# Performance work log

Hardware: AMD Instinct MI355X
Metric: run time of the kernel (lower is better)

## Reference

```python
import jax, jax.numpy as jnp
import numpy as np


def _find(parent, x):
    # chase parent pointers to the root (root = min-rank node of its component)
    return jax.lax.while_loop(lambda v: parent[v] != v, lambda v: parent[v], x)


def _pd0_single(fcol, src, dst):
    """0-dim persistence diagram for one filtration column.

    Semantics match TOGL.generate_persistence_diagram_dim0:
      - nodes are added in sorted order of fcol; birth(node) = its sorted rank
      - directed edge (u, v) merges components at step rank(v) iff rank(u) < rank(v)
      - elder rule: the component whose root has the larger rank dies
      - output row i = (birth=i, death) for the node of rank i (insertion order of
        the original dict is exactly rank order); death = inf for survivors.
    """
    n = fcol.shape[0]
    order = jnp.argsort(fcol)
    rank = jnp.zeros((n,), jnp.int32).at[order].set(jnp.arange(n, dtype=jnp.int32))
    a = rank[src]                      # rank-space endpoints
    b = rank[dst]
    valid = a < b                      # only edges whose source is already active fire
    w = jnp.where(valid, b, n)         # edge weight = step at which it fires
    perm = jnp.argsort(w)              # Kruskal order
    ea, eb, ev = a[perm], b[perm], valid[perm]

    def step(carry, e):
        parent, deaths = carry
        ia, ib, v = e
        ra = _find(parent, ia)
        rb = _find(parent, ib)
        merge = v & (ra != rb)
        elder = jnp.minimum(ra, rb)
        younger = jnp.maximum(ra, rb)
        deaths = deaths.at[younger].set(jnp.where(merge, ib.astype(deaths.dtype), deaths[younger]))
        parent = parent.at[younger].set(jnp.where(merge, elder, parent[younger]))
        # path compression at the two queried nodes
        parent = parent.at[ia].set(jnp.where(merge, elder, ra))
        parent = parent.at[ib].set(jnp.where(merge, elder, rb))
        return (parent, deaths), None

    parent0 = jnp.arange(n, dtype=jnp.int32)
    deaths0 = jnp.full((n,), jnp.inf, jnp.float32)
    (parent, deaths), _ = jax.lax.scan(step, (parent0, deaths0), (ea, eb, ev))
    births = jnp.arange(n, dtype=jnp.float32)
    return jnp.stack([births, deaths], axis=1)  # (n_nodes, 2)


def setup_inputs() -> dict:
    key = jax.random.key(0)
    k = jax.random.split(key, 6)
    N, F, H, NF, E = 20000, 1024, 2048, 4, 160000
    X = jax.random.normal(k[0], (N, F), jnp.float32)
    edge_index = jax.random.randint(k[1], (2, E), 0, N, jnp.int64)
    W1 = jax.random.normal(k[2], (F, H), jnp.float32) / np.sqrt(F)
    b1 = jax.random.normal(k[3], (H,), jnp.float32) * 0.01
    W2 = jax.random.normal(k[4], (H, NF), jnp.float32) / np.sqrt(H)
    b2 = jax.random.normal(k[5], (NF,), jnp.float32) * 0.01
    return {"X": X, "edge_index": edge_index, "W1": W1, "b1": b1, "W2": W2, "b2": b2}


def reference(X, edge_index, W1, b1, W2, b2):
    # filter_graph: Linear -> ReLU -> Linear
    filt = jnp.maximum(X @ W1 + b1, 0.0) @ W2 + b2            # (N, n_filtrations)
    src = edge_index[0].astype(jnp.int32)
    dst = edge_index[1].astype(jnp.int32)
    diagrams = jax.vmap(_pd0_single, in_axes=(1, None, None))(filt, src, dst)  # (NF, N, 2)
    return filt, diagrams
```

## Files before the change

### kernel.cpp

```cpp
#include <hip/hip_runtime.h>

typedef unsigned long long u64;
typedef unsigned int u32;
typedef unsigned short ushort_t;
typedef __attribute__((ext_vector_type(8))) short short8;
typedef __attribute__((ext_vector_type(4))) float fx4;

#define F_DIM 1024
#define H_DIM 2048
#define NFOUT 4
#define WS_W1T_OFF (1u << 20)

__device__ __forceinline__ ushort_t f2bf(float x)
{
    union { float f; u32 u; } c; c.f = x;
    u32 b = c.u;
    u32 r = b + 0x7FFFu + ((b >> 16) & 1u);
    return (ushort_t)(r >> 16);
}
__device__ __forceinline__ float bf2f(ushort_t h)
{
    union { u32 u; float f; } c; c.u = ((u32)h) << 16;
    return c.f;
}
__device__ __forceinline__ void split3(float x, ushort_t& u0, ushort_t& u1, ushort_t& u2)
{
    u0 = f2bf(x);
    float r1 = x - bf2f(u0);
    u1 = f2bf(r1);
    float r2 = r1 - bf2f(u1);
    u2 = f2bf(r2);
}

__global__ __launch_bounds__(256)
void k_w1split(const float* __restrict__ W1, ushort_t* __restrict__ w1t)
{
    __shared__ __align__(16) ushort_t LT[3][64][72];
    const int t = threadIdx.x;
    const int bk = blockIdx.x >> 5;
    const int bh = blockIdx.x & 31;
    const int k0 = bk * 64, h0 = bh * 64;
    const int kk = t >> 4, hb = (t & 15) * 4;
    #pragma unroll
    for (int j = 0; j < 4; j++) {
        int row = kk + j * 16;
        float4 v = *(const float4*)(W1 + (size_t)(k0 + row) * H_DIM + h0 + hb);
        float xs[4] = { v.x, v.y, v.z, v.w };
        #pragma unroll
        for (int c = 0; c < 4; c++) {
            ushort_t u0, u1, u2;
            split3(xs[c], u0, u1, u2);
            LT[0][hb + c][row] = u0;
            LT[1][hb + c][row] = u1;
            LT[2][hb + c][row] = u2;
        }
    }
    __syncthreads();
    const int hl = t >> 2, sg = t & 3;
    #pragma unroll
    for (int p = 0; p < 3; p++)
        #pragma unroll
        for (int q = 0; q < 2; q++) {
            int ks = sg * 16 + q * 8;
            *(short8*)(w1t + (size_t)p * (H_DIM * (size_t)F_DIM)
                       + (size_t)(h0 + hl) * F_DIM + k0 + ks) =
                *(const short8*)&LT[p][hl][ks];
        }
}

__device__ __forceinline__ fx4 mfma16(short8 a, short8 b, fx4 c)
{
    return __builtin_amdgcn_mfma_f32_16x16x32_bf16(a, b, c, 0, 0, 0);
}

#define AP_BYTES (3 * 64 * 128)
#define BP_BYTES (3 * 256 * 128)
#define SM_BYTES (AP_BYTES + BP_BYTES + 256 * 4 * 4)
#define HPITCH 261

__global__ __launch_bounds__(512, 2)
void k_filt_mfma(const float* __restrict__ X, const ushort_t* __restrict__ w1t,
                 const float* __restrict__ b1, const float* __restrict__ W2,
                 const float* __restrict__ b2, float* __restrict__ out, int N)
{
    extern __shared__ char smem[];
    char* Ac = smem;
    char* Bc = smem + AP_BYTES;
    float* W2s = (float*)(smem + AP_BYTES + BP_BYTES);
    float* hid = (float*)Bc;
    float* part = (float*)Ac;

    const int t = threadIdx.x;
    const int lane = t & 63;
    const int w = t >> 6;
    const int wr = (w & 1) * 32;
    const int wc = (w >> 1) * 64;
    const int r0 = blockIdx.x * 64;
    const int l15 = lane & 15, l4 = lane >> 4;

    const int arow = t >> 3;
    const int ak8  = (t & 7) * 8;
    const bool arow_ok = (r0 + arow) < N;
    const int brow = t >> 1;
    const int bseg = (t & 1) * 64;

    const int g2row = lane;
    const int g2nf  = w & 3;
    const int g2seg = w >> 2;

    float Afl[8];
    short8 Bv[12];
    fx4 acc[2][4];
    float pacc = 0.f;
    #pragma unroll
    for (int i = 0; i < 2; i++)
        #pragma unroll
        for (int j = 0; j < 4; j++) acc[i][j] = (fx4)(0.f);

    {
        if (arow_ok) {
            float4 v0 = *(const float4*)(X + (size_t)(r0 + arow) * F_DIM + ak8);
            float4 v1 = *(const float4*)(X + (size_t)(r0 + arow) * F_DIM + ak8 + 4);
            Afl[0] = v0.x; Afl[1] = v0.y; Afl[2] = v0.z; Afl[3] = v0.w;
            Afl[4] = v1.x; Afl[5] = v1.y; Afl[6] = v1.z; Afl[7] = v1.w;
        } else {
            #pragma unroll
            for (int j = 0; j < 8; j++) Afl[j] = 0.f;
        }
        #pragma unroll
        for (int p = 0; p < 3; p++)
            #pragma unroll
            for (int q = 0; q < 4; q++)
                Bv[p * 4 + q] = *(const short8*)(w1t + (size_t)p * (H_DIM * (size_t)F_DIM)
                                 + (size_t)brow * F_DIM + (bseg + q * 16) / 2);
    }

    for (int it = 0; it < 128; ++it) {
        const int hc = it >> 4, kc = it & 15;

        ushort_t s0[8], s1[8], s2[8];
        #pragma unroll
        for (int j = 0; j < 8; j++) split3(Afl[j], s0[j], s1[j], s2[j]);
        short8 Au0, Au1, Au2;
        #pragma unroll
        for (int j = 0; j < 8; j++) { Au0[j] = (short)s0[j]; Au1[j] = (short)s1[j]; Au2[j] = (short)s2[j]; }

        __syncthreads();

        {
            const int aswz = (arow & 7) << 4;
            const int abyte = (ak8 * 2);
            *(short8*)(Ac + 0 * 8192 + arow * 128 + (abyte ^ aswz)) = Au0;
            *(short8*)(Ac + 1 * 8192 + arow * 128 + (abyte ^ aswz)) = Au1;
            *(short8*)(Ac + 2 * 8192 + arow * 128 + (abyte ^ aswz)) = Au2;
            const int bswz = (brow & 7) << 4;
            #pragma unroll
            for (int p = 0; p < 3; p++)
                #pragma unroll
                for (int q = 0; q < 4; q++)
                    *(short8*)(Bc + p * 32768 + brow * 128 + ((bseg + q * 16) ^ bswz)) = Bv[p * 4 + q];
            if (kc == 0 && t < 256)
                *(float4*)&W2s[t * 4] = *(const float4*)(W2 + ((size_t)hc * 256 + t) * NFOUT);
        }

        if (it + 1 < 128) {
            const int hn = (it + 1) >> 4, kn = (it + 1) & 15;
            if (arow_ok) {
                float4 v0 = *(const float4*)(X + (size_t)(r0 + arow) * F_DIM + kn * 64 + ak8);
                float4 v1 = *(const float4*)(X + (size_t)(r0 + arow) * F_DIM + kn * 64 + ak8 + 4);
                Afl[0] = v0.x; Afl[1] = v0.y; Afl[2] = v0.z; Afl[3] = v0.w;
                Afl[4] = v1.x; Afl[5] = v1.y; Afl[6] = v1.z; Afl[7] = v1.w;
            }
            #pragma unroll
            for (int p = 0; p < 3; p++)
                #pragma unroll
                for (int q = 0; q < 4; q++)
                    Bv[p * 4 + q] = *(const short8*)(w1t + (size_t)p * (H_DIM * (size_t)F_DIM)
                                     + (size_t)(hn * 256 + brow) * F_DIM + kn * 64 + (bseg + q * 16) / 2);
        }

        __syncthreads();

        #pragma unroll
        for (int sub = 0; sub < 2; ++sub) {
            const int kb = sub * 64 + l4 * 16;
            const int sw = (l15 & 7) << 4;
            short8 a[2][3];
            #pragma unroll
            for (int rr = 0; rr < 2; ++rr) {
                const int row = wr + rr * 16 + l15;
                #pragma unroll
                for (int p = 0; p < 3; p++)
                    a[rr][p] = *(const short8*)(Ac + p * 8192 + row * 128 + (kb ^ sw));
            }
            #pragma unroll
            for (int cf = 0; cf < 4; ++cf) {
                const int hrow = wc + cf * 16 + l15;
                short8 bb0 = *(const short8*)(Bc + 0 * 32768 + hrow * 128 + (kb ^ sw));
                short8 bb1 = *(const short8*)(Bc + 1 * 32768 + hrow * 128 + (kb ^ sw));
                short8 bb2 = *(const short8*)(Bc + 2 * 32768 + hrow * 128 + (kb ^ sw));
                #pragma unroll
                for (int rr = 0; rr < 2; ++rr) {
                    fx4 c = acc[rr][cf];
                    c = mfma16(a[rr][0], bb0, c);
                    c = mfma16(a[rr][0], bb1, c);
                    c = mfma16(a[rr][1], bb0, c);
                    c = mfma16(a[rr][0], bb2, c);
                    c = mfma16(a[rr][1], bb1, c);
                    c = mfma16(a[rr][2], bb0, c);
                    acc[rr][cf] = c;
                }
            }
        }

        if (kc == 15) {
            __syncthreads();
            #pragma unroll
            for (int rr = 0; rr < 2; ++rr)
                #pragma unroll
                for (int cf = 0; cf < 4; ++cf) {
                    const int hl = wc + cf * 16 + l15;
                    const float bias1 = b1[hc * 256 + hl];
                    #pragma unroll
                    for (int g = 0; g < 4; g++) {
                        const int rl = wr + rr * 16 + l4 * 4 + g;
                        hid[rl * HPITCH + hl] = fmaxf(acc[rr][cf][g] + bias1, 0.f);
                    }
                    acc[rr][cf] = (fx4)(0.f);
                }
            __syncthreads();
            {
                const float* hp = hid + g2row * HPITCH + g2seg * 128;
                const int hb = g2seg * 128;
                #pragma unroll 16
                for (int j = 0; j < 128; j++)
                    pacc = fmaf(hp[j], W2s[(hb + j) * 4 + g2nf], pacc);
            }
        }
    }

    __syncthreads();
    part[g2row * 8 + g2nf * 2 + g2seg] = pacc;
    __syncthreads();
    if (t < 256) {
        const int row = t >> 2, nf = t & 3;
        const float s = part[row * 8 + nf * 2 + 0] + part[row * 8 + nf * 2 + 1];
        const int rg = r0 + row;
        if (rg < N) out[(size_t)rg * NFOUT + nf] = s + b2[nf];
    }
}

#define BM 64
#define BH 64
#define KCH 64
#define LROW 68

__global__ __launch_bounds__(256, 2)
void k_filt(const float* __restrict__ X, const float* __restrict__ W1,
            const float* __restrict__ b1, const float* __restrict__ W2,
            const float* __restrict__ b2, float* __restrict__ out, int N)
{
    __shared__ float Xs[KCH * LROW];
    __shared__ float Ws[KCH * LROW];
    __shared__ float W2s[BH * NFOUT];
    const int t = threadIdx.x;
    const int r0 = blockIdx.x * BM;
    const int tr = t >> 4, tc = t & 15;
    const int orow = t >> 2, onf = t & 3;
    float fchain = 0.0f;
    for (int hc = 0; hc < H_DIM; hc += BH) {
        float acc[4][4];
        #pragma unroll
        for (int i = 0; i < 4; i++)
            #pragma unroll
            for (int j = 0; j < 4; j++) acc[i][j] = 0.0f;
        for (int kc = 0; kc < F_DIM; kc += KCH) {
            {
                const int rowq = t >> 4, kkq = t & 15;
                float xv[4][4];
                #pragma unroll
                for (int j = 0; j < 4; j++) {
                    int r = r0 + rowq * 4 + j;
                    float4 v = (r < N) ? *(const float4*)(X + (size_t)r * F_DIM + kc + kkq * 4)
                                       : make_float4(0.f, 0.f, 0.f, 0.f);
                    xv[j][0] = v.x; xv[j][1] = v.y; xv[j][2] = v.z; xv[j][3] = v.w;
                }
                #pragma unroll
                for (int j = 0; j < 4; j++)
                    *(float4*)&Xs[(kkq * 4 + j) * LROW + rowq * 4] =
                        make_float4(xv[0][j], xv[1][j], xv[2][j], xv[3][j]);
            }
            {
                const int hq = t & 15;
                #pragma unroll
                for (int q = 0; q < 4; q++) {
                    int kk = (t >> 4) + q * 16;
                    *(float4*)&Ws[kk * LROW + hq * 4] =
                        *(const float4*)(W1 + (size_t)(kc + kk) * H_DIM + hc + hq * 4);
                }
            }
            __syncthreads();
            #pragma unroll 8
            for (int kk = 0; kk < KCH; kk++) {
                float4 xv = *(float4*)&Xs[kk * LROW + tr * 4];
                float4 wv = *(float4*)&Ws[kk * LROW + tc * 4];
                acc[0][0] = fmaf(xv.x, wv.x, acc[0][0]); acc[0][1] = fmaf(xv.x, wv.y, acc[0][1]);
                acc[0][2] = fmaf(xv.x, wv.z, acc[0][2]); acc[0][3] = fmaf(xv.x, wv.w, acc[0][3]);
                acc[1][0] = fmaf(xv.y, wv.x, acc[1][0]); acc[1][1] = fmaf(xv.y, wv.y, acc[1][1]);
                acc[1][2] = fmaf(xv.y, wv.z, acc[1][2]); acc[1][3] = fmaf(xv.y, wv.w, acc[1][3]);
                acc[2][0] = fmaf(xv.z, wv.x, acc[2][0]); acc[2][1] = fmaf(xv.z, wv.y, acc[2][1]);
                acc[2][2] = fmaf(xv.z, wv.z, acc[2][2]); acc[2][3] = fmaf(xv.z, wv.w, acc[2][3]);
                acc[3][0] = fmaf(xv.w, wv.x, acc[3][0]); acc[3][1] = fmaf(xv.w, wv.y, acc[3][1]);
                acc[3][2] = fmaf(xv.w, wv.z, acc[3][2]); acc[3][3] = fmaf(xv.w, wv.w, acc[3][3]);
            }
            __syncthreads();
        }
        {
            float4 bv = *(const float4*)(b1 + hc + tc * 4);
            #pragma unroll
            for (int i = 0; i < 4; i++) {
                float4 hv;
                hv.x = fmaxf(acc[i][0] + bv.x, 0.f);
                hv.y = fmaxf(acc[i][1] + bv.y, 0.f);
                hv.z = fmaxf(acc[i][2] + bv.z, 0.f);
                hv.w = fmaxf(acc[i][3] + bv.w, 0.f);
                *(float4*)&Ws[(tr * 4 + i) * LROW + tc * 4] = hv;
            }
            if (t < BH)
                *(float4*)&W2s[t * 4] = *(const float4*)(W2 + (size_t)(hc + t) * NFOUT);
        }
        __syncthreads();
        #pragma unroll 16
        for (int hh = 0; hh < BH; hh++)
            fchain = fmaf(Ws[orow * LROW + hh], W2s[hh * 4 + onf], fchain);
        __syncthreads();
    }
    {
        int r = r0 + orow;
        if (r < N) out[(size_t)r * NFOUT + onf] = fchain + b2[onf];
    }
}

__global__ void k_prep(u32* __restrict__ rank, int N)
{
    int g = blockIdx.x * blockDim.x + threadIdx.x;
    if (g < 4 * N) rank[g] = 0u;
}

#define JTILE 2048

__global__ __launch_bounds__(256)
void k_rank(const float* __restrict__ filt, u32* __restrict__ rank,
            int N, int nchunk)
{
    __shared__ float4 lds[JTILE];
    const int chunk = blockIdx.x % nchunk;
    const int jslice = blockIdx.x / nchunk;
    const int jt = jslice * JTILE;
    const int i = chunk * 256 + threadIdx.x;
    const bool iok = i < N;
    float4 vi = iok ? *(const float4*)(filt + (size_t)i * 4)
                    : make_float4(0.f, 0.f, 0.f, 0.f);
    for (int s = 0; s < JTILE; s += 256) {
        int j = jt + s + threadIdx.x;
        lds[s + threadIdx.x] = (j < N)
            ? *(const float4*)(filt + (size_t)j * 4)
            : make_float4(INFINITY, INFINITY, INFINITY, INFINITY);
    }
    __syncthreads();
    int c0 = 0, c1 = 0, c2 = 0, c3 = 0;
    #pragma unroll 4
    for (int jj = 0; jj < JTILE; jj++) {
        float4 vj = lds[jj];
        int j = jt + jj;
        bool jlt = j < i;
        c0 += (vj.x < vi.x) || (vj.x == vi.x && jlt);
        c1 += (vj.y < vi.y) || (vj.y == vi.y && jlt);
        c2 += (vj.z < vi.z) || (vj.z == vi.z && jlt);
        c3 += (vj.w < vi.w) || (vj.w == vi.w && jlt);
    }
    if (iok) {
        atomicAdd(&rank[0 * N + i], (u32)c0);
        atomicAdd(&rank[1 * N + i], (u32)c1);
        atomicAdd(&rank[2 * N + i], (u32)c2);
        atomicAdd(&rank[3 * N + i], (u32)c3);
    }
}

__device__ __forceinline__ u32 lds_aload(u32* p)
{
    return __hip_atomic_load(p, __ATOMIC_RELAXED, __HIP_MEMORY_SCOPE_WORKGROUP);
}

__device__ __forceinline__ u32 rep_walk32(u32* S, u32 u, u32 t, u32& sv_out)
{
    u32 sv = lds_aload(&S[u]);
    while ((sv >> 16) <= t) {
        u = sv & 0xFFFFu;
        sv = lds_aload(&S[u]);
    }
    sv_out = sv;
    return u;
}

__device__ void do_merge32(u32* S, u32 u, u32 v, u32 t)
{
    for (int guard = 0; guard < (1 << 22); guard++) {
        u32 svu, svv;
        u = rep_walk32(S, u, t, svu);
        v = rep_walk32(S, v, t, svv);
        if (u == v) return;
        if (u < v) { u32 tm = u; u = v; v = tm; u32 ts = svu; svu = svv; svv = ts; }
        u32 s = svu >> 16;
        if (s <= t) continue;
        u32 des = (t << 16) | v;
        u32 old = atomicCAS(&S[u], svu, des);
        if (old == svu) {
            if (s == 0xFFFFu) return;
            u = v; v = old & 0xFFFFu;
            t = s;
        }
    }
}

__global__ __launch_bounds__(1024, 1)
void k_merge4(const int* __restrict__ eidx, const u32* __restrict__ rank,
              float* __restrict__ dg, int N, int E)
{
    extern __shared__ u32 S[];
    const int f = blockIdx.x;
    const u32* rk = rank + (size_t)f * N;

    for (int u = threadIdx.x; u < N; u += blockDim.x)
        S[u] = (0xFFFFu << 16) | (u32)u;
    __syncthreads();

    for (int e = threadIdx.x; e < E; e += blockDim.x) {
        u32 a = rk[eidx[e]];
        u32 b = rk[eidx[E + e]];
        if (a < b) do_merge32(S, a, b, b);
    }
    __syncthreads();

    for (int r = threadIdx.x; r < N; r += blockDim.x) {
        u32 s = S[r] >> 16;
        float death = (s == 0xFFFFu) ? 3.0e38f : (float)s;
        dg[(size_t)f * N * 2 + (size_t)r * 2 + 0] = (float)r;
        dg[(size_t)f * N * 2 + (size_t)r * 2 + 1] = death;
    }
}

extern "C" void kernel_launch(void* const* d_in, const int* in_sizes, int n_in,
                              void* d_out, int out_size, void* d_ws, size_t ws_size,
                              hipStream_t stream)
{
    const float* X  = (const float*)d_in[0];
    const int*   EI = (const int*)d_in[1];
    const float* W1 = (const float*)d_in[2];
    const float* b1 = (const float*)d_in[3];
    const float* W2 = (const float*)d_in[4];
    const float* b2 = (const float*)d_in[5];
    const int N = in_sizes[0] / F_DIM;
    const int E = in_sizes[1] / 2;

    float* out = (float*)d_out;
    float* dg  = out + (size_t)N * NFOUT;
    u32* rank  = (u32*)d_ws;

    static bool attr_set = false;
    if (!attr_set) {
        (void)hipFuncSetAttribute((const void*)k_merge4,
                                  hipFuncAttributeMaxDynamicSharedMemorySize,
                                  160 * 1024);
        (void)hipFuncSetAttribute((const void*)k_filt_mfma,
                                  hipFuncAttributeMaxDynamicSharedMemorySize,
                                  160 * 1024);
        attr_set = true;
    }

    k_prep<<<(4 * N + 255) / 256, 256, 0, stream>>>(rank, N);

    const size_t w1t_need = (size_t)WS_W1T_OFF + 3ull * H_DIM * F_DIM * 2;
    if (ws_size >= w1t_need) {
        ushort_t* w1t = (ushort_t*)((char*)d_ws + WS_W1T_OFF);
        k_w1split<<<512, 256, 0, stream>>>(W1, w1t);
        k_filt_mfma<<<(N + 63) / 64, 512, SM_BYTES, stream>>>(X, w1t, b1, W2, b2, out, N);
    } else {
        k_filt<<<(N + BM - 1) / BM, 256, 0, stream>>>(X, W1, b1, W2, b2, out, N);
    }

    const int nchunk = (N + 255) / 256;
    const int njt    = (N + JTILE - 1) / JTILE;
    k_rank<<<nchunk * njt, 256, 0, stream>>>(out, rank, N, nchunk);
    k_merge4<<<4, 1024, (size_t)N * sizeof(u32), stream>>>(EI, rank, dg, N, E);
}
```

Before: 1.820 ms.

## Double row tile to 128 per block in split-bf16 MFMA filter GEMM

Each block of the 3-way split-bf16 MFMA GEMM now covers 128 rows of X instead of 64. Each wave computes a 64x64 output tile (4x4 MFMA fragments), so every W1 chunk staged in LDS is reused across twice as many rows and the grid is halved. The second layer now gives each thread a full 256-wide dot product per hidden chunk, which removes the cross-wave partial-sum reduction. The cost is more accumulator and A-fragment registers and a larger LDS footprint, which may lower occupancy against the launch bound of 2 blocks.

```diff
diff --git a/kernel.cpp b/kernel.cpp
--- a/kernel.cpp
+++ b/kernel.cpp
@@ -73,10 +73,11 @@
     return __builtin_amdgcn_mfma_f32_16x16x32_bf16(a, b, c, 0, 0, 0);
 }
 
-#define AP_BYTES (3 * 64 * 128)
+#define AP_BYTES (3 * 128 * 128)
 #define BP_BYTES (3 * 256 * 128)
-#define SM_BYTES (AP_BYTES + BP_BYTES + 256 * 4 * 4)
-#define HPITCH 261
+#define W2_OFF   (AP_BYTES + BP_BYTES)
+#define SM_BYTES (W2_OFF + 256 * 4 * 4)
+#define HPITCH 260
 
 __global__ __launch_bounds__(512, 2)
 void k_filt_mfma(const float* __restrict__ X, const ushort_t* __restrict__ w1t,
@@ -86,73 +87,78 @@
     extern __shared__ char smem[];
     char* Ac = smem;
     char* Bc = smem + AP_BYTES;
-    float* W2s = (float*)(smem + AP_BYTES + BP_BYTES);
-    float* hid = (float*)Bc;
-    float* part = (float*)Ac;
+    float* W2s = (float*)(smem + W2_OFF);
+    float* hid = (float*)smem;
 
     const int t = threadIdx.x;
     const int lane = t & 63;
     const int w = t >> 6;
-    const int wr = (w & 1) * 32;
-    const int wc = (w >> 1) * 64;
-    const int r0 = blockIdx.x * 64;
+    const int wr = (w >> 2) * 64;
+    const int wc = (w & 3) * 64;
+    const int r0 = blockIdx.x * 128;
     const int l15 = lane & 15, l4 = lane >> 4;
-
-    const int arow = t >> 3;
-    const int ak8  = (t & 7) * 8;
+    const int fsw = (l15 & 7) << 4;
+
+    const int arow = t >> 2;
+    const int aq   = (t & 3);
     const bool arow_ok = (r0 + arow) < N;
     const int brow = t >> 1;
     const int bseg = (t & 1) * 64;
 
-    const int g2row = lane;
-    const int g2nf  = w & 3;
-    const int g2seg = w >> 2;
-
-    float Afl[8];
+    const int orow = t >> 2;
+    const int onf  = t & 3;
+
+    float Afl[16];
     short8 Bv[12];
-    fx4 acc[2][4];
+    fx4 acc[4][4];
     float pacc = 0.f;
     #pragma unroll
-    for (int i = 0; i < 2; i++)
+    for (int i = 0; i < 4; i++)
         #pragma unroll
         for (int j = 0; j < 4; j++) acc[i][j] = (fx4)(0.f);
 
     {
         if (arow_ok) {
-            float4 v0 = *(const float4*)(X + (size_t)(r0 + arow) * F_DIM + ak8);
-            float4 v1 = *(const float4*)(X + (size_t)(r0 + arow) * F_DIM + ak8 + 4);
-            Afl[0] = v0.x; Afl[1] = v0.y; Afl[2] = v0.z; Afl[3] = v0.w;
-            Afl[4] = v1.x; Afl[5] = v1.y; Afl[6] = v1.z; Afl[7] = v1.w;
+            #pragma unroll
+            for (int q = 0; q < 4; q++) {
+                float4 v = *(const float4*)(X + (size_t)(r0 + arow) * F_DIM + aq * 16 + q * 4);
+                Afl[q * 4 + 0] = v.x; Afl[q * 4 + 1] = v.y;
+                Afl[q * 4 + 2] = v.z; Afl[q * 4 + 3] = v.w;
+            }
         } else {
             #pragma unroll
-            for (int j = 0; j < 8; j++) Afl[j] = 0.f;
+            for (int j = 0; j < 16; j++) Afl[j] = 0.f;
         }
         #pragma unroll
         for (int p = 0; p < 3; p++)
             #pragma unroll
             for (int q = 0; q < 4; q++)
                 Bv[p * 4 + q] = *(const short8*)(w1t + (size_t)p * (H_DIM * (size_t)F_DIM)
-                                 + (size_t)brow * F_DIM + (bseg + q * 16) / 2);
+                                 + (size_t)brow * F_DIM + bseg / 2 + q * 8);
     }
 
     for (int it = 0; it < 128; ++it) {
         const int hc = it >> 4, kc = it & 15;
 
-        ushort_t s0[8], s1[8], s2[8];
-        #pragma unroll
-        for (int j = 0; j < 8; j++) split3(Afl[j], s0[j], s1[j], s2[j]);
-        short8 Au0, Au1, Au2;
-        #pragma unroll
-        for (int j = 0; j < 8; j++) { Au0[j] = (short)s0[j]; Au1[j] = (short)s1[j]; Au2[j] = (short)s2[j]; }
+        ushort_t s0[16], s1[16], s2[16];
+        #pragma unroll
+        for (int j = 0; j < 16; j++) split3(Afl[j], s0[j], s1[j], s2[j]);
 
         __syncthreads();
 
         {
             const int aswz = (arow & 7) << 4;
-            const int abyte = (ak8 * 2);
-            *(short8*)(Ac + 0 * 8192 + arow * 128 + (abyte ^ aswz)) = Au0;
-            *(short8*)(Ac + 1 * 8192 + arow * 128 + (abyte ^ aswz)) = Au1;
-            *(short8*)(Ac + 2 * 8192 + arow * 128 + (abyte ^ aswz)) = Au2;
+            #pragma unroll
+            for (int p = 0; p < 3; p++) {
+                const ushort_t* sp = (p == 0) ? s0 : (p == 1) ? s1 : s2;
+                #pragma unroll
+                for (int h = 0; h < 2; h++) {
+                    short8 pk;
+                    #pragma unroll
+                    for (int i = 0; i < 8; i++) pk[i] = (short)sp[h * 8 + i];
+                    *(short8*)(Ac + p * 16384 + arow * 128 + ((aq * 32 + h * 16) ^ aswz)) = pk;
+                }
+            }
             const int bswz = (brow & 7) << 4;
             #pragma unroll
             for (int p = 0; p < 3; p++)
@@ -166,17 +172,19 @@
         if (it + 1 < 128) {
             const int hn = (it + 1) >> 4, kn = (it + 1) & 15;
             if (arow_ok) {
-                float4 v0 = *(const float4*)(X + (size_t)(r0 + arow) * F_DIM + kn * 64 + ak8);
-                float4 v1 = *(const float4*)(X + (size_t)(r0 + arow) * F_DIM + kn * 64 + ak8 + 4);
-                Afl[0] = v0.x; Afl[1] = v0.y; Afl[2] = v0.z; Afl[3] = v0.w;
-                Afl[4] = v1.x; Afl[5] = v1.y; Afl[6] = v1.z; Afl[7] = v1.w;
+                #pragma unroll
+                for (int q = 0; q < 4; q++) {
+                    float4 v = *(const float4*)(X + (size_t)(r0 + arow) * F_DIM + kn * 64 + aq * 16 + q * 4);
+                    Afl[q * 4 + 0] = v.x; Afl[q * 4 + 1] = v.y;
+                    Afl[q * 4 + 2] = v.z; Afl[q * 4 + 3] = v.w;
+                }
             }
             #pragma unroll
             for (int p = 0; p < 3; p++)
                 #pragma unroll
                 for (int q = 0; q < 4; q++)
                     Bv[p * 4 + q] = *(const short8*)(w1t + (size_t)p * (H_DIM * (size_t)F_DIM)
-                                     + (size_t)(hn * 256 + brow) * F_DIM + kn * 64 + (bseg + q * 16) / 2);
+                                     + (size_t)(hn * 256 + brow) * F_DIM + kn * 64 + bseg / 2 + q * 8);
         }
 
         __syncthreads();
@@ -184,30 +192,29 @@
         #pragma unroll
         for (int sub = 0; sub < 2; ++sub) {
             const int kb = sub * 64 + l4 * 16;
-            const int sw = (l15 & 7) << 4;
-            short8 a[2][3];
-            #pragma unroll
-            for (int rr = 0; rr < 2; ++rr) {
-                const int row = wr + rr * 16 + l15;
-                #pragma unroll
-                for (int p = 0; p < 3; p++)
-                    a[rr][p] = *(const short8*)(Ac + p * 8192 + row * 128 + (kb ^ sw));
-            }
+            short8 b[4][3];
             #pragma unroll
             for (int cf = 0; cf < 4; ++cf) {
                 const int hrow = wc + cf * 16 + l15;
-                short8 bb0 = *(const short8*)(Bc + 0 * 32768 + hrow * 128 + (kb ^ sw));
-                short8 bb1 = *(const short8*)(Bc + 1 * 32768 + hrow * 128 + (kb ^ sw));
-                short8 bb2 = *(const short8*)(Bc + 2 * 32768 + hrow * 128 + (kb ^ sw));
-                #pragma unroll
-                for (int rr = 0; rr < 2; ++rr) {
+                #pragma unroll
+                for (int p = 0; p < 3; p++)
+                    b[cf][p] = *(const short8*)(Bc + p * 32768 + hrow * 128 + (kb ^ fsw));
+            }
+            #pragma unroll
+            for (int rr = 0; rr < 4; ++rr) {
+                const int row = wr + rr * 16 + l15;
+                short8 a0 = *(const short8*)(Ac + 0 * 16384 + row * 128 + (kb ^ fsw));
+                short8 a1 = *(const short8*)(Ac + 1 * 16384 + row * 128 + (kb ^ fsw));
+                short8 a2 = *(const short8*)(Ac + 2 * 16384 + row * 128 + (kb ^ fsw));
+                #pragma unroll
+                for (int cf = 0; cf < 4; ++cf) {
                     fx4 c = acc[rr][cf];
-                    c = mfma16(a[rr][0], bb0, c);
-                    c = mfma16(a[rr][0], bb1, c);
-                    c = mfma16(a[rr][1], bb0, c);
-                    c = mfma16(a[rr][0], bb2, c);
-                    c = mfma16(a[rr][1], bb1, c);
-                    c = mfma16(a[rr][2], bb0, c);
+                    c = mfma16(a0, b[cf][0], c);
+                    c = mfma16(a0, b[cf][1], c);
+                    c = mfma16(a1, b[cf][0], c);
+                    c = mfma16(a0, b[cf][2], c);
+                    c = mfma16(a1, b[cf][1], c);
+                    c = mfma16(a2, b[cf][0], c);
                     acc[rr][cf] = c;
                 }
             }
@@ -216,7 +223,7 @@
         if (kc == 15) {
             __syncthreads();
             #pragma unroll
-            for (int rr = 0; rr < 2; ++rr)
+            for (int rr = 0; rr < 4; ++rr)
                 #pragma unroll
                 for (int cf = 0; cf < 4; ++cf) {
                     const int hl = wc + cf * 16 + l15;
@@ -230,23 +237,17 @@
                 }
             __syncthreads();
             {
-                const float* hp = hid + g2row * HPITCH + g2seg * 128;
-                const int hb = g2seg * 128;
+                const float* hp = hid + orow * HPITCH;
                 #pragma unroll 16
-                for (int j = 0; j < 128; j++)
-                    pacc = fmaf(hp[j], W2s[(hb + j) * 4 + g2nf], pacc);
-            }
-        }
-    }
-
-    __syncthreads();
-    part[g2row * 8 + g2nf * 2 + g2seg] = pacc;
-    __syncthreads();
-    if (t < 256) {
-        const int row = t >> 2, nf = t & 3;
-        const float s = part[row * 8 + nf * 2 + 0] + part[row * 8 + nf * 2 + 1];
-        const int rg = r0 + row;
-        if (rg < N) out[(size_t)rg * NFOUT + nf] = s + b2[nf];
+                for (int j = 0; j < 256; j++)
+                    pacc = fmaf(hp[j], W2s[j * 4 + onf], pacc);
+            }
+        }
+    }
+
+    {
+        const int rg = r0 + orow;
+        if (rg < N) out[(size_t)rg * NFOUT + onf] = pacc + b2[onf];
     }
 }
 
@@ -484,7 +485,7 @@
     if (ws_size >= w1t_need) {
         ushort_t* w1t = (ushort_t*)((char*)d_ws + WS_W1T_OFF);
         k_w1split<<<512, 256, 0, stream>>>(W1, w1t);
-        k_filt_mfma<<<(N + 63) / 64, 512, SM_BYTES, stream>>>(X, w1t, b1, W2, b2, out, N);
+        k_filt_mfma<<<(N + 127) / 128, 512, SM_BYTES, stream>>>(X, w1t, b1, W2, b2, out, N);
     } else {
         k_filt<<<(N + BM - 1) / BM, 256, 0, stream>>>(X, W1, b1, W2, b2, out, N);
     }
```

Result: faster. 1.603 ms (-11.9%).
